# Optimization experiments

Hardware: AMD Instinct MI355X
Metric: run time of the kernel (lower is better)

## Reference

```python
import jax, jax.numpy as jnp
import numpy as np

V, E, H, O = 32000, 300, 300, 9   # vocab, embed_dim, hidden, n_tags
B, T = 128, 512                   # batch, seq_len


def setup_inputs() -> dict:
    key = jax.random.key(0)
    ks = jax.random.split(key, 10)
    w = lambda k, shape: (jax.random.normal(k, shape, jnp.float32) * 0.05)
    return {
        "x": jax.random.randint(ks[0], (B, T), 0, V),
        "emb_table": w(ks[1], (V, E)),
        "W_ih_f": w(ks[2], (4 * H, E)),   # torch gate order: i, f, g, o
        "W_hh_f": w(ks[3], (4 * H, H)),
        "b_f": w(ks[4], (4 * H,)),        # b_ih + b_hh fused (mathematically identical)
        "W_ih_b": w(ks[5], (4 * H, E)),
        "W_hh_b": w(ks[6], (4 * H, H)),
        "b_b": w(ks[7], (4 * H,)),
        "W_lin": w(ks[8], (O, 2 * H)),
        "b_lin": w(ks[9], (O,)),
    }


def _lstm_dir(emb, W_ih, W_hh, b, reverse):
    # Pre-project inputs once (time-batched GEMM), scan only the recurrence.
    xp = jnp.einsum("bte,ge->btg", emb, W_ih) + b      # [B,T,4H]
    xp = jnp.swapaxes(xp, 0, 1)                         # [T,B,4H]
    Bv = emb.shape[0]
    Hv = W_hh.shape[1]
    z = jnp.zeros((Bv, Hv), emb.dtype)

    def step(carry, xt):
        h, c = carry
        gates = xt + h @ W_hh.T                          # [B,4H]
        i, f, g, o = jnp.split(gates, 4, axis=-1)
        c = jax.nn.sigmoid(f) * c + jax.nn.sigmoid(i) * jnp.tanh(g)
        h = jax.nn.sigmoid(o) * jnp.tanh(c)
        return (h, c), h

    _, hs = jax.lax.scan(step, (z, z), xp, reverse=reverse)
    return jnp.swapaxes(hs, 0, 1)                        # [B,T,H]


def reference(x, emb_table, W_ih_f, W_hh_f, b_f, W_ih_b, W_hh_b, b_b, W_lin, b_lin):
    emb = emb_table[x]                                   # [B,T,E]
    hf = _lstm_dir(emb, W_ih_f, W_hh_f, b_f, reverse=False)
    hb = _lstm_dir(emb, W_ih_b, W_hh_b, b_b, reverse=True)
    out = jnp.concatenate([hf, hb], axis=-1) @ W_lin.T + b_lin  # [B,T,O]
    return jax.nn.softmax(out, axis=-1)
```

## Files before the change

kernel.cpp:

```cpp
#include <hip/hip_runtime.h>
#include <stdint.h>

#define Tn 512
#define Bn 128
#define NTOK (Bn*Tn)
#define En 300
#define Hn 300
#define On 9
#define LDK 328
#define HS 60
#define NSL 5
#define NCH 8
#define MC 16
#define GLD 244
#define NBLK (2*NCH*NSL)
#define NTHR 960

#define HXW 304
#define HXSLOT (Bn*HXW)
#define HXDIR (2*HXSLOT)

typedef short s4v __attribute__((ext_vector_type(4)));
typedef short s8v __attribute__((ext_vector_type(8)));
typedef float f4v __attribute__((ext_vector_type(4)));

__device__ unsigned short g_hcat[NTOK * 2 * Hn];
__device__ unsigned int   g_hx[2 * HXDIR];

__device__ inline float b2f(unsigned short u){ unsigned v = ((unsigned)u) << 16; float f; __builtin_memcpy(&f, &v, 4); return f; }
__device__ inline unsigned short f2b(float f){ unsigned u; __builtin_memcpy(&u, &f, 4); u = u + 0x7fffu + ((u >> 16) & 1u); return (unsigned short)(u >> 16); }
__device__ inline float sigf(float x){ return 1.f / (1.f + __expf(-x)); }
__device__ inline float tanh_f(float x){ return 2.f / (1.f + __expf(-2.f * x)) - 1.f; }

__device__ inline void bar_lgkm(){ asm volatile("s_waitcnt lgkmcnt(0)\n\ts_barrier" ::: "memory"); }

__global__ __launch_bounds__(256) void k_zero()
{
    const int i = blockIdx.x * 256 + threadIdx.x;
    const int stride = gridDim.x * 256;
    for (int j = i; j < 2 * HXDIR; j += stride) g_hx[j] = 0xFFFFu;
}

__global__ __launch_bounds__(NTHR, 4) void k_lstm(
    const int* __restrict__ x, const float* __restrict__ emb,
    const float* __restrict__ W_ih_f, const float* __restrict__ W_hh_f, const float* __restrict__ b_f,
    const float* __restrict__ W_ih_b, const float* __restrict__ W_hh_b, const float* __restrict__ b_b)
{
    const int bi    = blockIdx.x;
    const int dir   = bi / (NCH * NSL);
    const int rem   = bi % (NCH * NSL);
    const int chunk = rem / NSL;
    const int slice = rem % NSL;
    const int j0    = slice * HS;
    const int b0    = chunk * MC;

    const float* Wih  = dir ? W_ih_b : W_ih_f;
    const float* Whh  = dir ? W_hh_b : W_hh_f;
    const float* bias = dir ? b_b    : b_f;
    unsigned int* hxd = g_hx + dir * HXDIR;

    __shared__ __align__(16) unsigned short Aemb[2][MC * LDK];
    __shared__ __align__(16) unsigned short Hb[MC * LDK];
    __shared__ __align__(16) float Gsm[MC * GLD];
    __shared__ unsigned short Xl[MC * Tn];

    const int tid  = threadIdx.x;
    const int lane = tid & 63;
    const int wid  = tid >> 6;
    const int n0   = wid * 16;
    const int kq   = (lane >> 4) * 8;

    const int nloc = n0 + (lane & 15);
    const int q    = nloc / HS;
    const int jjn  = nloc % HS;
    const int grow = q * Hn + j0 + jjn;
    s8v bih[10], bhh[10];
#pragma unroll
    for (int kc = 0; kc < 10; kc++) {
        int kb = kc * 32 + kq;
        s8v fi = {0,0,0,0,0,0,0,0}, fh = {0,0,0,0,0,0,0,0};
#pragma unroll
        for (int j = 0; j < 8; j++) {
            int k = kb + j;
            if (k < En) {
                fi[j] = (short)f2b(Wih[grow * En + k]);
                fh[j] = (short)f2b(Whh[grow * Hn + k]);
            }
        }
        bih[kc] = fi; bhh[kc] = fh;
    }

    const int ebl = tid / HS;
    const int ejj = tid % HS;
    const float bi_i = bias[0 * Hn + j0 + ejj];
    const float bi_f = bias[1 * Hn + j0 + ejj];
    const float bi_g = bias[2 * Hn + j0 + ejj];
    const float bi_o = bias[3 * Hn + j0 + ejj];
    float creg = 0.f;
    const bool pub = ((ejj & 1) == 0);

    int goffA[4], loffA[4];
#pragma unroll
    for (int j = 0; j < 4; j++) {
        int i  = tid + j * NTHR;
        int r  = i / (4 * HS);
        int c2 = i - r * (4 * HS);
        int c  = (c2 < j0) ? c2 : (c2 + HS);
        goffA[j] = (b0 + r) * HXW + c;
        loffA[j] = r * LDK + c;
    }

    {
        const int t0 = dir ? (Tn - 1) : 0;
        for (int i = tid; i < MC * 80; i += NTHR) {
            int r = i / 80, c = i - r * 80;
            s4v v = {0, 0, 0, 0};
            if (c < 75) {
                int xi = x[(b0 + r) * Tn + t0];
                float4 f = *(const float4*)(emb + (size_t)xi * En + c * 4);
                v[0] = (short)f2b(f.x); v[1] = (short)f2b(f.y);
                v[2] = (short)f2b(f.z); v[3] = (short)f2b(f.w);
            }
            *(s4v*)&Aemb[0][r * LDK + c * 4] = v;
        }
        for (int i = tid; i < MC * Tn; i += NTHR) {
            int r = i >> 9, tt = i & (Tn - 1);
            Xl[i] = (unsigned short)x[(b0 + r) * Tn + tt];
        }
        if (tid < MC * 20) {
            int r = tid / 20, c = 300 + (tid % 20);
            Hb[r * LDK + c] = 0;
        }
        __syncthreads();
    }

#pragma unroll 1
    for (int s = 0; s < Tn; s++) {
        const int t   = dir ? (Tn - 1 - s) : s;
        const int cur = s & 1, nxt = cur ^ 1;

        const unsigned int* hsrc = hxd + (s & 1) * HXSLOT;
        unsigned int pv0, pv1, pv2, pv3;
        if (s) {
            pv0 = __hip_atomic_load(hsrc + goffA[0], __ATOMIC_RELAXED, __HIP_MEMORY_SCOPE_AGENT);
            pv1 = __hip_atomic_load(hsrc + goffA[1], __ATOMIC_RELAXED, __HIP_MEMORY_SCOPE_AGENT);
            pv2 = __hip_atomic_load(hsrc + goffA[2], __ATOMIC_RELAXED, __HIP_MEMORY_SCOPE_AGENT);
            pv3 = __hip_atomic_load(hsrc + goffA[3], __ATOMIC_RELAXED, __HIP_MEMORY_SCOPE_AGENT);
        }

        f4v acc = {0.f, 0.f, 0.f, 0.f};
        {
            const unsigned short* abase = &Aemb[cur][(lane & 15) * LDK + kq];
#pragma unroll
            for (int kc = 0; kc < 10; kc++) {
                s8v a = *(const s8v*)(abase + kc * 32);
                acc = __builtin_amdgcn_mfma_f32_16x16x32_bf16(a, bih[kc], acc, 0, 0, 0);
            }
        }

        f4v acc2 = {0.f, 0.f, 0.f, 0.f};
        if (s) {
            const unsigned tgt = (unsigned)(s - 1);
            for (;;) {
                unsigned bad = ((pv0 ^ tgt) | (pv1 ^ tgt) | (pv2 ^ tgt) | (pv3 ^ tgt)) & 0xffffu;
                if (!bad) break;
                pv0 = __hip_atomic_load(hsrc + goffA[0], __ATOMIC_RELAXED, __HIP_MEMORY_SCOPE_AGENT);
                pv1 = __hip_atomic_load(hsrc + goffA[1], __ATOMIC_RELAXED, __HIP_MEMORY_SCOPE_AGENT);
                pv2 = __hip_atomic_load(hsrc + goffA[2], __ATOMIC_RELAXED, __HIP_MEMORY_SCOPE_AGENT);
                pv3 = __hip_atomic_load(hsrc + goffA[3], __ATOMIC_RELAXED, __HIP_MEMORY_SCOPE_AGENT);
            }
            Hb[loffA[0]] = (unsigned short)(pv0 >> 16);
            Hb[loffA[1]] = (unsigned short)(pv1 >> 16);
            Hb[loffA[2]] = (unsigned short)(pv2 >> 16);
            Hb[loffA[3]] = (unsigned short)(pv3 >> 16);
        }

        float4 pf[2];
        const bool do_pf = (s + 1 < Tn);
        if (do_pf) {
            const int tn1 = dir ? (Tn - 2 - s) : (s + 1);
#pragma unroll
            for (int k = 0; k < 2; k++) {
                int i = tid + k * NTHR;
                if (i < MC * 80) {
                    int r = i / 80, c = i - r * 80;
                    if (c < 75) {
                        int xi = (int)Xl[(r << 9) + tn1];
                        pf[k] = *(const float4*)(emb + (size_t)xi * En + c * 4);
                    }
                }
            }
        }

        if (s) {
            bar_lgkm();

            const unsigned short* abase = &Hb[(lane & 15) * LDK + kq];
#pragma unroll
            for (int kc = 0; kc < 10; kc += 2) {
                s8v a0 = *(const s8v*)(abase + kc * 32);
                s8v a1 = *(const s8v*)(abase + (kc + 1) * 32);
                acc  = __builtin_amdgcn_mfma_f32_16x16x32_bf16(a0, bhh[kc],     acc,  0, 0, 0);
                acc2 = __builtin_amdgcn_mfma_f32_16x16x32_bf16(a1, bhh[kc + 1], acc2, 0, 0, 0);
            }
        }

        {
            int col   = n0 + (lane & 15);
            int rbase = (lane >> 4) * 4;
#pragma unroll
            for (int r2 = 0; r2 < 4; r2++) Gsm[(rbase + r2) * GLD + col] = acc[r2] + acc2[r2];
        }
        bar_lgkm();

        {
            float gi  = Gsm[ebl * GLD + 0 * HS + ejj] + bi_i;
            float gf  = Gsm[ebl * GLD + 1 * HS + ejj] + bi_f;
            float gg2 = Gsm[ebl * GLD + 2 * HS + ejj] + bi_g;
            float go  = Gsm[ebl * GLD + 3 * HS + ejj] + bi_o;
            float iv = sigf(gi), fv = sigf(gf), gv = tanh_f(gg2), ov = sigf(go);
            creg = fv * creg + iv * gv;
            float h = ov * tanh_f(creg);
            unsigned hb16 = (unsigned)f2b(h);

            Hb[ebl * LDK + j0 + ejj] = (unsigned short)hb16;

            __hip_atomic_store(hxd + ((s + 1) & 1) * HXSLOT + (b0 + ebl) * HXW + (j0 + ejj),
                               (hb16 << 16) | (unsigned)s,
                               __ATOMIC_RELAXED, __HIP_MEMORY_SCOPE_AGENT);

            float hn = __shfl_down(h, 1);
            if (pub) {
                unsigned pkt = hb16 | ((unsigned)f2b(hn) << 16);
                __hip_atomic_store((unsigned int*)g_hcat
                                       + (((size_t)((b0 + ebl) * Tn + t)) * (2 * Hn) + dir * Hn + j0 + ejj) / 2,
                                   pkt, __ATOMIC_RELAXED, __HIP_MEMORY_SCOPE_AGENT);
            }
        }

        if (do_pf) {
#pragma unroll
            for (int k = 0; k < 2; k++) {
                int i = tid + k * NTHR;
                if (i < MC * 80) {
                    int r = i / 80, c = i - r * 80;
                    s4v v = {0, 0, 0, 0};
                    if (c < 75) {
                        v[0] = (short)f2b(pf[k].x); v[1] = (short)f2b(pf[k].y);
                        v[2] = (short)f2b(pf[k].z); v[3] = (short)f2b(pf[k].w);
                    }
                    *(s4v*)&Aemb[nxt][r * LDK + c * 4] = v;
                }
            }
        }
        bar_lgkm();
    }
}

__global__ __launch_bounds__(256) void k_out(
    const float* __restrict__ W_lin, const float* __restrict__ b_lin, float* __restrict__ out)
{
    __shared__ float Wl[On * 2 * Hn];
    __shared__ float bl[On];
    const int tid = threadIdx.x;
    for (int i = tid; i < On * 2 * Hn; i += 256) Wl[i] = W_lin[i];
    if (tid < On) bl[tid] = b_lin[tid];
    __syncthreads();

    const int lane = tid & 63;
    const int w    = tid >> 6;
    const int wg   = blockIdx.x * 4 + w;
    for (int it = 0; it < 16; it++) {
        const int p = wg * 16 + it;
        const unsigned int* rowd = (const unsigned int*)(g_hcat + (size_t)p * (2 * Hn));
        float part[On];
#pragma unroll
        for (int o = 0; o < On; o++) part[o] = 0.f;
#pragma unroll
        for (int c = 0; c < 5; c++) {
            int k = lane + 64 * c;
            if (k < Hn) {
                unsigned v2 = rowd[k];
                float vlo = b2f((unsigned short)(v2 & 0xffffu));
                float vhi = b2f((unsigned short)(v2 >> 16));
#pragma unroll
                for (int o = 0; o < On; o++)
                    part[o] += vlo * Wl[o * (2 * Hn) + 2 * k] + vhi * Wl[o * (2 * Hn) + 2 * k + 1];
            }
        }
#pragma unroll
        for (int off = 32; off >= 1; off >>= 1) {
#pragma unroll
            for (int o = 0; o < On; o++) part[o] += __shfl_xor(part[o], off, 64);
        }
        if (lane == 0) {
            float lg[On];
            float m = -1e30f;
#pragma unroll
            for (int o = 0; o < On; o++) { lg[o] = part[o] + bl[o]; m = fmaxf(m, lg[o]); }
            float ssum = 0.f;
#pragma unroll
            for (int o = 0; o < On; o++) { lg[o] = __expf(lg[o] - m); ssum += lg[o]; }
            float inv = 1.f / ssum;
#pragma unroll
            for (int o = 0; o < On; o++) out[(size_t)p * On + o] = lg[o] * inv;
        }
    }
}

extern "C" void kernel_launch(void* const* d_in, const int* in_sizes, int n_in,
                              void* d_out, int out_size, void* d_ws, size_t ws_size,
                              hipStream_t stream)
{
    (void)in_sizes; (void)n_in; (void)out_size; (void)d_ws; (void)ws_size;
    const int* x = (const int*)d_in[0];
    const float* emb   = (const float*)d_in[1];
    const float* Wih_f = (const float*)d_in[2];
    const float* Whh_f = (const float*)d_in[3];
    const float* bf    = (const float*)d_in[4];
    const float* Wih_b = (const float*)d_in[5];
    const float* Whh_b = (const float*)d_in[6];
    const float* bb    = (const float*)d_in[7];
    const float* Wlin  = (const float*)d_in[8];
    const float* blin  = (const float*)d_in[9];
    float* out = (float*)d_out;

    k_zero<<<128, 256, 0, stream>>>();

    void* args[] = {
        (void*)&x, (void*)&emb,
        (void*)&Wih_f, (void*)&Whh_f, (void*)&bf,
        (void*)&Wih_b, (void*)&Whh_b, (void*)&bb
    };
    hipLaunchCooperativeKernel((const void*)k_lstm, dim3(NBLK), dim3(NTHR), args, 0, stream);

    k_out<<<1024, 256, 0, stream>>>(Wlin, blin, out);
}
```

Measured before the change: 2.307 ms.

## Process two batch chunks per LSTM block, halving the grid

Each block now handles two 16-row batch chunks (A and B) with a shared weight-register set, so the grid goes from 80 to 40 blocks and occupancy hint drops to 2. The two chunks' MFMA chains are interleaved to hide latency, and the LDS token cache and double-buffered embedding are replaced by per-step global token loads and single-buffered embedding per chunk. The aim is to reduce the number of communicating blocks and amortise per-step sync over twice the work. In exchange each step has serialized gate phases with extra barriers and longer per-block critical path.

```diff
diff --git a/kernel.cpp b/kernel.cpp
--- a/kernel.cpp
+++ b/kernel.cpp
@@ -11,9 +11,10 @@
 #define HS 60
 #define NSL 5
 #define NCH 8
+#define NPAIR 4
 #define MC 16
 #define GLD 244
-#define NBLK (2*NCH*NSL)
+#define NBLK (2*NPAIR*NSL)
 #define NTHR 960
 
 #define HXW 304
@@ -41,28 +42,30 @@
     for (int j = i; j < 2 * HXDIR; j += stride) g_hx[j] = 0xFFFFu;
 }
 
-__global__ __launch_bounds__(NTHR, 4) void k_lstm(
+__global__ __launch_bounds__(NTHR, 2) void k_lstm(
     const int* __restrict__ x, const float* __restrict__ emb,
     const float* __restrict__ W_ih_f, const float* __restrict__ W_hh_f, const float* __restrict__ b_f,
     const float* __restrict__ W_ih_b, const float* __restrict__ W_hh_b, const float* __restrict__ b_b)
 {
     const int bi    = blockIdx.x;
-    const int dir   = bi / (NCH * NSL);
-    const int rem   = bi % (NCH * NSL);
-    const int chunk = rem / NSL;
+    const int dir   = bi / (NPAIR * NSL);
+    const int rem   = bi % (NPAIR * NSL);
+    const int pair  = rem / NSL;
     const int slice = rem % NSL;
     const int j0    = slice * HS;
-    const int b0    = chunk * MC;
+    const int b0A   = (2 * pair)     * MC;
+    const int b0B   = (2 * pair + 1) * MC;
 
     const float* Wih  = dir ? W_ih_b : W_ih_f;
     const float* Whh  = dir ? W_hh_b : W_hh_f;
     const float* bias = dir ? b_b    : b_f;
     unsigned int* hxd = g_hx + dir * HXDIR;
 
-    __shared__ __align__(16) unsigned short Aemb[2][MC * LDK];
-    __shared__ __align__(16) unsigned short Hb[MC * LDK];
+    __shared__ __align__(16) unsigned short AembA[MC * LDK];
+    __shared__ __align__(16) unsigned short AembB[MC * LDK];
+    __shared__ __align__(16) unsigned short HbA[MC * LDK];
+    __shared__ __align__(16) unsigned short HbB[MC * LDK];
     __shared__ __align__(16) float Gsm[MC * GLD];
-    __shared__ unsigned short Xl[MC * Tn];
 
     const int tid  = threadIdx.x;
     const int lane = tid & 63;
@@ -96,97 +99,125 @@
     const float bi_f = bias[1 * Hn + j0 + ejj];
     const float bi_g = bias[2 * Hn + j0 + ejj];
     const float bi_o = bias[3 * Hn + j0 + ejj];
-    float creg = 0.f;
+    float cregA = 0.f, cregB = 0.f;
     const bool pub = ((ejj & 1) == 0);
 
-    int goffA[4], loffA[4];
+    int goffA[4], goffB[4], loff[4];
 #pragma unroll
     for (int j = 0; j < 4; j++) {
         int i  = tid + j * NTHR;
         int r  = i / (4 * HS);
         int c2 = i - r * (4 * HS);
         int c  = (c2 < j0) ? c2 : (c2 + HS);
-        goffA[j] = (b0 + r) * HXW + c;
-        loffA[j] = r * LDK + c;
+        goffA[j] = (b0A + r) * HXW + c;
+        goffB[j] = (b0B + r) * HXW + c;
+        loff[j]  = r * LDK + c;
     }
 
     {
         const int t0 = dir ? (Tn - 1) : 0;
         for (int i = tid; i < MC * 80; i += NTHR) {
             int r = i / 80, c = i - r * 80;
-            s4v v = {0, 0, 0, 0};
+            s4v vA = {0,0,0,0}, vB = {0,0,0,0};
             if (c < 75) {
-                int xi = x[(b0 + r) * Tn + t0];
-                float4 f = *(const float4*)(emb + (size_t)xi * En + c * 4);
-                v[0] = (short)f2b(f.x); v[1] = (short)f2b(f.y);
-                v[2] = (short)f2b(f.z); v[3] = (short)f2b(f.w);
-            }
-            *(s4v*)&Aemb[0][r * LDK + c * 4] = v;
-        }
-        for (int i = tid; i < MC * Tn; i += NTHR) {
-            int r = i >> 9, tt = i & (Tn - 1);
-            Xl[i] = (unsigned short)x[(b0 + r) * Tn + tt];
+                int xiA = x[(b0A + r) * Tn + t0];
+                int xiB = x[(b0B + r) * Tn + t0];
+                float4 fA = *(const float4*)(emb + (size_t)xiA * En + c * 4);
+                float4 fB = *(const float4*)(emb + (size_t)xiB * En + c * 4);
+                vA[0] = (short)f2b(fA.x); vA[1] = (short)f2b(fA.y);
+                vA[2] = (short)f2b(fA.z); vA[3] = (short)f2b(fA.w);
+                vB[0] = (short)f2b(fB.x); vB[1] = (short)f2b(fB.y);
+                vB[2] = (short)f2b(fB.z); vB[3] = (short)f2b(fB.w);
+            }
+            *(s4v*)&AembA[r * LDK + c * 4] = vA;
+            *(s4v*)&AembB[r * LDK + c * 4] = vB;
         }
         if (tid < MC * 20) {
             int r = tid / 20, c = 300 + (tid % 20);
-            Hb[r * LDK + c] = 0;
+            HbA[r * LDK + c] = 0;
+            HbB[r * LDK + c] = 0;
         }
         __syncthreads();
     }
 
 #pragma unroll 1
     for (int s = 0; s < Tn; s++) {
-        const int t   = dir ? (Tn - 1 - s) : s;
-        const int cur = s & 1, nxt = cur ^ 1;
-
-        const unsigned int* hsrc = hxd + (s & 1) * HXSLOT;
-        unsigned int pv0, pv1, pv2, pv3;
-        if (s) {
-            pv0 = __hip_atomic_load(hsrc + goffA[0], __ATOMIC_RELAXED, __HIP_MEMORY_SCOPE_AGENT);
-            pv1 = __hip_atomic_load(hsrc + goffA[1], __ATOMIC_RELAXED, __HIP_MEMORY_SCOPE_AGENT);
-            pv2 = __hip_atomic_load(hsrc + goffA[2], __ATOMIC_RELAXED, __HIP_MEMORY_SCOPE_AGENT);
-            pv3 = __hip_atomic_load(hsrc + goffA[3], __ATOMIC_RELAXED, __HIP_MEMORY_SCOPE_AGENT);
-        }
-
-        f4v acc = {0.f, 0.f, 0.f, 0.f};
-        {
-            const unsigned short* abase = &Aemb[cur][(lane & 15) * LDK + kq];
-#pragma unroll
-            for (int kc = 0; kc < 10; kc++) {
-                s8v a = *(const s8v*)(abase + kc * 32);
-                acc = __builtin_amdgcn_mfma_f32_16x16x32_bf16(a, bih[kc], acc, 0, 0, 0);
-            }
-        }
-
-        f4v acc2 = {0.f, 0.f, 0.f, 0.f};
-        if (s) {
-            const unsigned tgt = (unsigned)(s - 1);
-            for (;;) {
-                unsigned bad = ((pv0 ^ tgt) | (pv1 ^ tgt) | (pv2 ^ tgt) | (pv3 ^ tgt)) & 0xffffu;
-                if (!bad) break;
-                pv0 = __hip_atomic_load(hsrc + goffA[0], __ATOMIC_RELAXED, __HIP_MEMORY_SCOPE_AGENT);
-                pv1 = __hip_atomic_load(hsrc + goffA[1], __ATOMIC_RELAXED, __HIP_MEMORY_SCOPE_AGENT);
-                pv2 = __hip_atomic_load(hsrc + goffA[2], __ATOMIC_RELAXED, __HIP_MEMORY_SCOPE_AGENT);
-                pv3 = __hip_atomic_load(hsrc + goffA[3], __ATOMIC_RELAXED, __HIP_MEMORY_SCOPE_AGENT);
-            }
-            Hb[loffA[0]] = (unsigned short)(pv0 >> 16);
-            Hb[loffA[1]] = (unsigned short)(pv1 >> 16);
-            Hb[loffA[2]] = (unsigned short)(pv2 >> 16);
-            Hb[loffA[3]] = (unsigned short)(pv3 >> 16);
-        }
-
-        float4 pf[2];
+        const int t = dir ? (Tn - 1 - s) : s;
+
+        int xtA[2], xtB[2];
         const bool do_pf = (s + 1 < Tn);
         if (do_pf) {
             const int tn1 = dir ? (Tn - 2 - s) : (s + 1);
+#pragma unroll
+            for (int k = 0; k < 2; k++) {
+                int i = tid + k * NTHR;
+                if (i < MC * 80) {
+                    int r = i / 80;
+                    xtA[k] = x[(b0A + r) * Tn + tn1];
+                    xtB[k] = x[(b0B + r) * Tn + tn1];
+                }
+            }
+        }
+
+        f4v accA = {0.f,0.f,0.f,0.f}, accB = {0.f,0.f,0.f,0.f};
+        {
+            const unsigned short* aA = &AembA[(lane & 15) * LDK + kq];
+            const unsigned short* aB = &AembB[(lane & 15) * LDK + kq];
+#pragma unroll
+            for (int kc = 0; kc < 10; kc++) {
+                accA = __builtin_amdgcn_mfma_f32_16x16x32_bf16(*(const s8v*)(aA + kc * 32), bih[kc], accA, 0, 0, 0);
+                accB = __builtin_amdgcn_mfma_f32_16x16x32_bf16(*(const s8v*)(aB + kc * 32), bih[kc], accB, 0, 0, 0);
+            }
+        }
+
+        if (s) {
+            const unsigned tgt = (unsigned)(s - 1);
+            const unsigned int* hsrc = hxd + (s & 1) * HXSLOT;
+            unsigned int pb0, pb1, pb2, pb3, pa0, pa1, pa2, pa3;
+            pb0 = __hip_atomic_load(hsrc + goffB[0], __ATOMIC_RELAXED, __HIP_MEMORY_SCOPE_AGENT);
+            pb1 = __hip_atomic_load(hsrc + goffB[1], __ATOMIC_RELAXED, __HIP_MEMORY_SCOPE_AGENT);
+            pb2 = __hip_atomic_load(hsrc + goffB[2], __ATOMIC_RELAXED, __HIP_MEMORY_SCOPE_AGENT);
+            pb3 = __hip_atomic_load(hsrc + goffB[3], __ATOMIC_RELAXED, __HIP_MEMORY_SCOPE_AGENT);
+            pa0 = __hip_atomic_load(hsrc + goffA[0], __ATOMIC_RELAXED, __HIP_MEMORY_SCOPE_AGENT);
+            pa1 = __hip_atomic_load(hsrc + goffA[1], __ATOMIC_RELAXED, __HIP_MEMORY_SCOPE_AGENT);
+            pa2 = __hip_atomic_load(hsrc + goffA[2], __ATOMIC_RELAXED, __HIP_MEMORY_SCOPE_AGENT);
+            pa3 = __hip_atomic_load(hsrc + goffA[3], __ATOMIC_RELAXED, __HIP_MEMORY_SCOPE_AGENT);
+            for (;;) {
+                unsigned bad = ((pa0 ^ tgt) | (pa1 ^ tgt) | (pa2 ^ tgt) | (pa3 ^ tgt)) & 0xffffu;
+                if (!bad) break;
+                pa0 = __hip_atomic_load(hsrc + goffA[0], __ATOMIC_RELAXED, __HIP_MEMORY_SCOPE_AGENT);
+                pa1 = __hip_atomic_load(hsrc + goffA[1], __ATOMIC_RELAXED, __HIP_MEMORY_SCOPE_AGENT);
+                pa2 = __hip_atomic_load(hsrc + goffA[2], __ATOMIC_RELAXED, __HIP_MEMORY_SCOPE_AGENT);
+                pa3 = __hip_atomic_load(hsrc + goffA[3], __ATOMIC_RELAXED, __HIP_MEMORY_SCOPE_AGENT);
+            }
+            for (;;) {
+                unsigned bad = ((pb0 ^ tgt) | (pb1 ^ tgt) | (pb2 ^ tgt) | (pb3 ^ tgt)) & 0xffffu;
+                if (!bad) break;
+                pb0 = __hip_atomic_load(hsrc + goffB[0], __ATOMIC_RELAXED, __HIP_MEMORY_SCOPE_AGENT);
+                pb1 = __hip_atomic_load(hsrc + goffB[1], __ATOMIC_RELAXED, __HIP_MEMORY_SCOPE_AGENT);
+                pb2 = __hip_atomic_load(hsrc + goffB[2], __ATOMIC_RELAXED, __HIP_MEMORY_SCOPE_AGENT);
+                pb3 = __hip_atomic_load(hsrc + goffB[3], __ATOMIC_RELAXED, __HIP_MEMORY_SCOPE_AGENT);
+            }
+            HbA[loff[0]] = (unsigned short)(pa0 >> 16);
+            HbA[loff[1]] = (unsigned short)(pa1 >> 16);
+            HbA[loff[2]] = (unsigned short)(pa2 >> 16);
+            HbA[loff[3]] = (unsigned short)(pa3 >> 16);
+            HbB[loff[0]] = (unsigned short)(pb0 >> 16);
+            HbB[loff[1]] = (unsigned short)(pb1 >> 16);
+            HbB[loff[2]] = (unsigned short)(pb2 >> 16);
+            HbB[loff[3]] = (unsigned short)(pb3 >> 16);
+        }
+
+        float4 pfA[2], pfB[2];
+        if (do_pf) {
 #pragma unroll
             for (int k = 0; k < 2; k++) {
                 int i = tid + k * NTHR;
                 if (i < MC * 80) {
                     int r = i / 80, c = i - r * 80;
                     if (c < 75) {
-                        int xi = (int)Xl[(r << 9) + tn1];
-                        pf[k] = *(const float4*)(emb + (size_t)xi * En + c * 4);
+                        pfA[k] = *(const float4*)(emb + (size_t)xtA[k] * En + c * 4);
+                        pfB[k] = *(const float4*)(emb + (size_t)xtB[k] * En + c * 4);
                     }
                 }
             }
@@ -195,45 +226,65 @@
         if (s) {
             bar_lgkm();
 
-            const unsigned short* abase = &Hb[(lane & 15) * LDK + kq];
-#pragma unroll
-            for (int kc = 0; kc < 10; kc += 2) {
-                s8v a0 = *(const s8v*)(abase + kc * 32);
-                s8v a1 = *(const s8v*)(abase + (kc + 1) * 32);
-                acc  = __builtin_amdgcn_mfma_f32_16x16x32_bf16(a0, bhh[kc],     acc,  0, 0, 0);
-                acc2 = __builtin_amdgcn_mfma_f32_16x16x32_bf16(a1, bhh[kc + 1], acc2, 0, 0, 0);
-            }
-        }
-
-        {
-            int col   = n0 + (lane & 15);
-            int rbase = (lane >> 4) * 4;
-#pragma unroll
-            for (int r2 = 0; r2 < 4; r2++) Gsm[(rbase + r2) * GLD + col] = acc[r2] + acc2[r2];
-        }
+            const unsigned short* hA = &HbA[(lane & 15) * LDK + kq];
+            const unsigned short* hB = &HbB[(lane & 15) * LDK + kq];
+#pragma unroll
+            for (int kc = 0; kc < 10; kc++) {
+                accA = __builtin_amdgcn_mfma_f32_16x16x32_bf16(*(const s8v*)(hA + kc * 32), bhh[kc], accA, 0, 0, 0);
+                accB = __builtin_amdgcn_mfma_f32_16x16x32_bf16(*(const s8v*)(hB + kc * 32), bhh[kc], accB, 0, 0, 0);
+            }
+        }
+
+        const int col   = n0 + (lane & 15);
+        const int rbase = (lane >> 4) * 4;
+
+#pragma unroll
+        for (int r2 = 0; r2 < 4; r2++) Gsm[(rbase + r2) * GLD + col] = accA[r2];
         bar_lgkm();
-
         {
             float gi  = Gsm[ebl * GLD + 0 * HS + ejj] + bi_i;
             float gf  = Gsm[ebl * GLD + 1 * HS + ejj] + bi_f;
             float gg2 = Gsm[ebl * GLD + 2 * HS + ejj] + bi_g;
             float go  = Gsm[ebl * GLD + 3 * HS + ejj] + bi_o;
             float iv = sigf(gi), fv = sigf(gf), gv = tanh_f(gg2), ov = sigf(go);
-            creg = fv * creg + iv * gv;
-            float h = ov * tanh_f(creg);
+            cregA = fv * cregA + iv * gv;
+            float h = ov * tanh_f(cregA);
             unsigned hb16 = (unsigned)f2b(h);
-
-            Hb[ebl * LDK + j0 + ejj] = (unsigned short)hb16;
-
-            __hip_atomic_store(hxd + ((s + 1) & 1) * HXSLOT + (b0 + ebl) * HXW + (j0 + ejj),
+            HbA[ebl * LDK + j0 + ejj] = (unsigned short)hb16;
+            __hip_atomic_store(hxd + ((s + 1) & 1) * HXSLOT + (b0A + ebl) * HXW + (j0 + ejj),
                                (hb16 << 16) | (unsigned)s,
                                __ATOMIC_RELAXED, __HIP_MEMORY_SCOPE_AGENT);
-
             float hn = __shfl_down(h, 1);
             if (pub) {
                 unsigned pkt = hb16 | ((unsigned)f2b(hn) << 16);
                 __hip_atomic_store((unsigned int*)g_hcat
-                                       + (((size_t)((b0 + ebl) * Tn + t)) * (2 * Hn) + dir * Hn + j0 + ejj) / 2,
+                                       + (((size_t)((b0A + ebl) * Tn + t)) * (2 * Hn) + dir * Hn + j0 + ejj) / 2,
+                                   pkt, __ATOMIC_RELAXED, __HIP_MEMORY_SCOPE_AGENT);
+            }
+        }
+        bar_lgkm();
+
+#pragma unroll
+        for (int r2 = 0; r2 < 4; r2++) Gsm[(rbase + r2) * GLD + col] = accB[r2];
+        bar_lgkm();
+        {
+            float gi  = Gsm[ebl * GLD + 0 * HS + ejj] + bi_i;
+            float gf  = Gsm[ebl * GLD + 1 * HS + ejj] + bi_f;
+            float gg2 = Gsm[ebl * GLD + 2 * HS + ejj] + bi_g;
+            float go  = Gsm[ebl * GLD + 3 * HS + ejj] + bi_o;
+            float iv = sigf(gi), fv = sigf(gf), gv = tanh_f(gg2), ov = sigf(go);
+            cregB = fv * cregB + iv * gv;
+            float h = ov * tanh_f(cregB);
+            unsigned hb16 = (unsigned)f2b(h);
+            HbB[ebl * LDK + j0 + ejj] = (unsigned short)hb16;
+            __hip_atomic_store(hxd + ((s + 1) & 1) * HXSLOT + (b0B + ebl) * HXW + (j0 + ejj),
+                               (hb16 << 16) | (unsigned)s,
+                               __ATOMIC_RELAXED, __HIP_MEMORY_SCOPE_AGENT);
+            float hn = __shfl_down(h, 1);
+            if (pub) {
+                unsigned pkt = hb16 | ((unsigned)f2b(hn) << 16);
+                __hip_atomic_store((unsigned int*)g_hcat
+                                       + (((size_t)((b0B + ebl) * Tn + t)) * (2 * Hn) + dir * Hn + j0 + ejj) / 2,
                                    pkt, __ATOMIC_RELAXED, __HIP_MEMORY_SCOPE_AGENT);
             }
         }
@@ -244,12 +295,15 @@
                 int i = tid + k * NTHR;
                 if (i < MC * 80) {
                     int r = i / 80, c = i - r * 80;
-                    s4v v = {0, 0, 0, 0};
+                    s4v vA = {0,0,0,0}, vB = {0,0,0,0};
                     if (c < 75) {
-                        v[0] = (short)f2b(pf[k].x); v[1] = (short)f2b(pf[k].y);
-                        v[2] = (short)f2b(pf[k].z); v[3] = (short)f2b(pf[k].w);
+                        vA[0] = (short)f2b(pfA[k].x); vA[1] = (short)f2b(pfA[k].y);
+                        vA[2] = (short)f2b(pfA[k].z); vA[3] = (short)f2b(pfA[k].w);
+                        vB[0] = (short)f2b(pfB[k].x); vB[1] = (short)f2b(pfB[k].y);
+                        vB[2] = (short)f2b(pfB[k].z); vB[3] = (short)f2b(pfB[k].w);
                     }
-                    *(s4v*)&Aemb[nxt][r * LDK + c * 4] = v;
+                    *(s4v*)&AembA[r * LDK + c * 4] = vA;
+                    *(s4v*)&AembB[r * LDK + c * 4] = vB;
                 }
             }
         }
```

Result: slower. 6.903 ms (+199.2%).

## Interleave gate columns to compute LSTM cell in registers and pack h exchange

Applied to the files above, without the earlier changes.

Reorders the W_hh/W_ih weight columns so each MFMA tile holds all four gates of a hidden unit interleaved. The cell update can then be assembled in registers with xor shuffles, which removes the Gsm shared-memory staging buffer and one block barrier per timestep. The cross-block hidden-state exchange now uses 64-bit words carrying two bf16 values plus a step tag, which halves the polled global loads and stores. The second accumulator chain is dropped, so the MFMA dependency chain is longer and the shuffles add some ALU work.

```diff
diff --git a/kernel.cpp b/kernel.cpp
--- a/kernel.cpp
+++ b/kernel.cpp
@@ -12,20 +12,19 @@
 #define NSL 5
 #define NCH 8
 #define MC 16
-#define GLD 244
 #define NBLK (2*NCH*NSL)
 #define NTHR 960
 
-#define HXW 304
-#define HXSLOT (Bn*HXW)
-#define HXDIR (2*HXSLOT)
+#define HXWQ 152
+#define HXSLOTQ (Bn*HXWQ)
+#define HXDIRQ (2*HXSLOTQ)
 
 typedef short s4v __attribute__((ext_vector_type(4)));
 typedef short s8v __attribute__((ext_vector_type(8)));
 typedef float f4v __attribute__((ext_vector_type(4)));
 
 __device__ unsigned short g_hcat[NTOK * 2 * Hn];
-__device__ unsigned int   g_hx[2 * HXDIR];
+__device__ unsigned long long g_hx[2 * HXDIRQ];
 
 __device__ inline float b2f(unsigned short u){ unsigned v = ((unsigned)u) << 16; float f; __builtin_memcpy(&f, &v, 4); return f; }
 __device__ inline unsigned short f2b(float f){ unsigned u; __builtin_memcpy(&u, &f, 4); u = u + 0x7fffu + ((u >> 16) & 1u); return (unsigned short)(u >> 16); }
@@ -38,7 +37,7 @@
 {
     const int i = blockIdx.x * 256 + threadIdx.x;
     const int stride = gridDim.x * 256;
-    for (int j = i; j < 2 * HXDIR; j += stride) g_hx[j] = 0xFFFFu;
+    for (int j = i; j < 2 * HXDIRQ; j += stride) g_hx[j] = 0xFFFFFFFFFFFFFFFFull;
 }
 
 __global__ __launch_bounds__(NTHR, 4) void k_lstm(
@@ -57,11 +56,10 @@
     const float* Wih  = dir ? W_ih_b : W_ih_f;
     const float* Whh  = dir ? W_hh_b : W_hh_f;
     const float* bias = dir ? b_b    : b_f;
-    unsigned int* hxd = g_hx + dir * HXDIR;
+    unsigned long long* hxq = g_hx + (size_t)dir * HXDIRQ;
 
     __shared__ __align__(16) unsigned short Aemb[2][MC * LDK];
     __shared__ __align__(16) unsigned short Hb[MC * LDK];
-    __shared__ __align__(16) float Gsm[MC * GLD];
     __shared__ unsigned short Xl[MC * Tn];
 
     const int tid  = threadIdx.x;
@@ -71,9 +69,9 @@
     const int kq   = (lane >> 4) * 8;
 
     const int nloc = n0 + (lane & 15);
-    const int q    = nloc / HS;
-    const int jjn  = nloc % HS;
-    const int grow = q * Hn + j0 + jjn;
+    const int gq   = nloc & 3;
+    const int uq   = nloc >> 2;
+    const int grow = gq * Hn + j0 + uq;
     s8v bih[10], bhh[10];
 #pragma unroll
     for (int kc = 0; kc < 10; kc++) {
@@ -90,24 +88,26 @@
         bih[kc] = fi; bhh[kc] = fh;
     }
 
-    const int ebl = tid / HS;
-    const int ejj = tid % HS;
-    const float bi_i = bias[0 * Hn + j0 + ejj];
-    const float bi_f = bias[1 * Hn + j0 + ejj];
-    const float bi_g = bias[2 * Hn + j0 + ejj];
-    const float bi_o = bias[3 * Hn + j0 + ejj];
+    const int crow = 4 * (lane >> 4) + (lane & 3);
+    const int cu   = (lane >> 2) & 3;
+    const int cj   = j0 + 4 * wid + cu;
+    const float bi_i = bias[0 * Hn + cj];
+    const float bi_f = bias[1 * Hn + cj];
+    const float bi_g = bias[2 * Hn + cj];
+    const float bi_o = bias[3 * Hn + cj];
     float creg = 0.f;
-    const bool pub = ((ejj & 1) == 0);
-
-    int goffA[4], loffA[4];
-#pragma unroll
-    for (int j = 0; j < 4; j++) {
-        int i  = tid + j * NTHR;
-        int r  = i / (4 * HS);
-        int c2 = i - r * (4 * HS);
-        int c  = (c2 < j0) ? c2 : (c2 + HS);
-        goffA[j] = (b0 + r) * HXW + c;
-        loffA[j] = r * LDK + c;
+    const bool pub = ((cu & 1) == 0);
+
+    int goffA[2], loffA[2];
+#pragma unroll
+    for (int jj = 0; jj < 2; jj++) {
+        int i  = tid + jj * NTHR;
+        int r  = i / 120;
+        int cq = i - r * 120;
+        int c  = 2 * cq;
+        c = (c < j0) ? c : (c + HS);
+        goffA[jj] = (b0 + r) * HXWQ + (c >> 1);
+        loffA[jj] = (r * LDK + c) >> 1;
     }
 
     {
@@ -139,15 +139,6 @@
         const int t   = dir ? (Tn - 1 - s) : s;
         const int cur = s & 1, nxt = cur ^ 1;
 
-        const unsigned int* hsrc = hxd + (s & 1) * HXSLOT;
-        unsigned int pv0, pv1, pv2, pv3;
-        if (s) {
-            pv0 = __hip_atomic_load(hsrc + goffA[0], __ATOMIC_RELAXED, __HIP_MEMORY_SCOPE_AGENT);
-            pv1 = __hip_atomic_load(hsrc + goffA[1], __ATOMIC_RELAXED, __HIP_MEMORY_SCOPE_AGENT);
-            pv2 = __hip_atomic_load(hsrc + goffA[2], __ATOMIC_RELAXED, __HIP_MEMORY_SCOPE_AGENT);
-            pv3 = __hip_atomic_load(hsrc + goffA[3], __ATOMIC_RELAXED, __HIP_MEMORY_SCOPE_AGENT);
-        }
-
         f4v acc = {0.f, 0.f, 0.f, 0.f};
         {
             const unsigned short* abase = &Aemb[cur][(lane & 15) * LDK + kq];
@@ -158,21 +149,19 @@
             }
         }
 
-        f4v acc2 = {0.f, 0.f, 0.f, 0.f};
         if (s) {
             const unsigned tgt = (unsigned)(s - 1);
+            const unsigned long long* hsrc = hxq + (size_t)(s & 1) * HXSLOTQ;
+            unsigned long long p0, p1;
+            p0 = __hip_atomic_load(hsrc + goffA[0], __ATOMIC_RELAXED, __HIP_MEMORY_SCOPE_AGENT);
+            p1 = __hip_atomic_load(hsrc + goffA[1], __ATOMIC_RELAXED, __HIP_MEMORY_SCOPE_AGENT);
             for (;;) {
-                unsigned bad = ((pv0 ^ tgt) | (pv1 ^ tgt) | (pv2 ^ tgt) | (pv3 ^ tgt)) & 0xffffu;
-                if (!bad) break;
-                pv0 = __hip_atomic_load(hsrc + goffA[0], __ATOMIC_RELAXED, __HIP_MEMORY_SCOPE_AGENT);
-                pv1 = __hip_atomic_load(hsrc + goffA[1], __ATOMIC_RELAXED, __HIP_MEMORY_SCOPE_AGENT);
-                pv2 = __hip_atomic_load(hsrc + goffA[2], __ATOMIC_RELAXED, __HIP_MEMORY_SCOPE_AGENT);
-                pv3 = __hip_atomic_load(hsrc + goffA[3], __ATOMIC_RELAXED, __HIP_MEMORY_SCOPE_AGENT);
-            }
-            Hb[loffA[0]] = (unsigned short)(pv0 >> 16);
-            Hb[loffA[1]] = (unsigned short)(pv1 >> 16);
-            Hb[loffA[2]] = (unsigned short)(pv2 >> 16);
-            Hb[loffA[3]] = (unsigned short)(pv3 >> 16);
+                if (((unsigned)p0 == tgt) & ((unsigned)p1 == tgt)) break;
+                p0 = __hip_atomic_load(hsrc + goffA[0], __ATOMIC_RELAXED, __HIP_MEMORY_SCOPE_AGENT);
+                p1 = __hip_atomic_load(hsrc + goffA[1], __ATOMIC_RELAXED, __HIP_MEMORY_SCOPE_AGENT);
+            }
+            ((unsigned int*)Hb)[loffA[0]] = (unsigned int)(p0 >> 32);
+            ((unsigned int*)Hb)[loffA[1]] = (unsigned int)(p1 >> 32);
         }
 
         float4 pf[2];
@@ -197,43 +186,49 @@
 
             const unsigned short* abase = &Hb[(lane & 15) * LDK + kq];
 #pragma unroll
-            for (int kc = 0; kc < 10; kc += 2) {
-                s8v a0 = *(const s8v*)(abase + kc * 32);
-                s8v a1 = *(const s8v*)(abase + (kc + 1) * 32);
-                acc  = __builtin_amdgcn_mfma_f32_16x16x32_bf16(a0, bhh[kc],     acc,  0, 0, 0);
-                acc2 = __builtin_amdgcn_mfma_f32_16x16x32_bf16(a1, bhh[kc + 1], acc2, 0, 0, 0);
-            }
-        }
-
+            for (int kc = 0; kc < 10; kc++) {
+                s8v a = *(const s8v*)(abase + kc * 32);
+                acc = __builtin_amdgcn_mfma_f32_16x16x32_bf16(a, bhh[kc], acc, 0, 0, 0);
+            }
+        }
+
+        float vi, vf2, vg, vo;
         {
-            int col   = n0 + (lane & 15);
-            int rbase = (lane >> 4) * 4;
-#pragma unroll
-            for (int r2 = 0; r2 < 4; r2++) Gsm[(rbase + r2) * GLD + col] = acc[r2] + acc2[r2];
-        }
-        bar_lgkm();
+            const bool q0 = (lane & 1) != 0;
+            const bool q1 = (lane & 2) != 0;
+            float a0 = acc[0], a1 = acc[1], a2 = acc[2], a3 = acc[3];
+            float s0 = __shfl_xor(a1, 1), s1 = __shfl_xor(a0, 1);
+            float s2 = __shfl_xor(a3, 1), s3 = __shfl_xor(a2, 1);
+            float b0v = q0 ? s0 : a0;
+            float b1v = q0 ? a1 : s1;
+            float b2v = q0 ? s2 : a2;
+            float b3v = q0 ? a3 : s3;
+            s0 = __shfl_xor(b2v, 2); s1 = __shfl_xor(b3v, 2);
+            s2 = __shfl_xor(b0v, 2); s3 = __shfl_xor(b1v, 2);
+            vi  = q1 ? s0 : b0v;
+            vf2 = q1 ? s1 : b1v;
+            vg  = q1 ? b2v : s2;
+            vo  = q1 ? b3v : s3;
+        }
 
         {
-            float gi  = Gsm[ebl * GLD + 0 * HS + ejj] + bi_i;
-            float gf  = Gsm[ebl * GLD + 1 * HS + ejj] + bi_f;
-            float gg2 = Gsm[ebl * GLD + 2 * HS + ejj] + bi_g;
-            float go  = Gsm[ebl * GLD + 3 * HS + ejj] + bi_o;
-            float iv = sigf(gi), fv = sigf(gf), gv = tanh_f(gg2), ov = sigf(go);
-            creg = fv * creg + iv * gv;
+            float gi  = vi  + bi_i;
+            float gf  = vf2 + bi_f;
+            float gg2 = vg  + bi_g;
+            float go  = vo  + bi_o;
+            float ivv = sigf(gi), fv = sigf(gf), gv = tanh_f(gg2), ov = sigf(go);
+            creg = fv * creg + ivv * gv;
             float h = ov * tanh_f(creg);
             unsigned hb16 = (unsigned)f2b(h);
-
-            Hb[ebl * LDK + j0 + ejj] = (unsigned short)hb16;
-
-            __hip_atomic_store(hxd + ((s + 1) & 1) * HXSLOT + (b0 + ebl) * HXW + (j0 + ejj),
-                               (hb16 << 16) | (unsigned)s,
-                               __ATOMIC_RELAXED, __HIP_MEMORY_SCOPE_AGENT);
-
-            float hn = __shfl_down(h, 1);
+            float hn = __shfl_down(h, 4);
             if (pub) {
                 unsigned pkt = hb16 | ((unsigned)f2b(hn) << 16);
+                ((unsigned int*)Hb)[(crow * LDK + cj) >> 1] = pkt;
+                __hip_atomic_store(hxq + (size_t)((s + 1) & 1) * HXSLOTQ + (b0 + crow) * HXWQ + (cj >> 1),
+                                   ((unsigned long long)pkt << 32) | (unsigned long long)(unsigned)s,
+                                   __ATOMIC_RELAXED, __HIP_MEMORY_SCOPE_AGENT);
                 __hip_atomic_store((unsigned int*)g_hcat
-                                       + (((size_t)((b0 + ebl) * Tn + t)) * (2 * Hn) + dir * Hn + j0 + ejj) / 2,
+                                       + (((size_t)((b0 + crow) * Tn + t)) * (2 * Hn) + dir * Hn + cj) / 2,
                                    pkt, __ATOMIC_RELAXED, __HIP_MEMORY_SCOPE_AGENT);
             }
         }
```

New measurement: 2.176 ms. -5.7%, faster.
